# Kernel optimization log

Measured on AMD Instinct MI355X. Metric: run time of the kernel, lower is better.

Reference implementation:

```python
import jax, jax.numpy as jnp
import numpy as np

TEMP = 0.05            # self.temp
NUM_INSTANCES = 16     # self.num_instances


def _l2norm(x):
    return x / jnp.linalg.norm(x, axis=-1, keepdims=True)


def setup_inputs() -> dict:
    key = jax.random.key(0)
    ks = jax.random.split(key, 6)
    B, D, N, K, NDATA = 256, 2048, 32768, 8192, 100000
    inputs = jax.random.normal(ks[0], (B, D), jnp.float32)
    # memory bank rows are kept unit-norm by the momentum update; init normalized
    features = _l2norm(jax.random.normal(ks[1], (N, D), jnp.float32))
    kmeans_centeroids = jax.random.normal(ks[2], (K, D), jnp.float32)
    targets = jax.random.randint(ks[3], (B,), 0, N)
    kmeans_pids = jax.random.randint(ks[4], (NDATA,), 0, K)
    indexes = jax.random.randint(ks[5], (B,), 0, NDATA)
    return {"inputs": inputs, "features": features,
            "kmeans_centeroids": kmeans_centeroids, "targets": targets,
            "kmeans_pids": kmeans_pids, "indexes": indexes, "neg_size": 20}


def reference(inputs, features, kmeans_centeroids, targets, kmeans_pids,
              indexes, neg_size):
    B = inputs.shape[0]
    K = kmeans_centeroids.shape[0]
    x = _l2norm(inputs)                                   # F.normalize(inputs, dim=1)
    outputs = x @ features.T                              # CM.forward: [B, N]
    finch_pos = jnp.take_along_axis(outputs, targets[:, None], axis=1)  # [B,1]
    kmeans_score = x @ kmeans_centeroids.T                # [B, K]
    batch_kmeans_pids = kmeans_pids[indexes]              # [B]
    # scatter_(-2) own kmeans cluster, then take top-neg_size negatives
    masked = jax.lax.stop_gradient(kmeans_score)          # detach().clone()
    masked = masked.at[jnp.arange(B), batch_kmeans_pids].set(-2.0)
    _, sel_ind_neg = jax.lax.top_k(masked, neg_size)      # [B, neg_size]
    kmeans_chosen_neg = jnp.take_along_axis(kmeans_score, sel_ind_neg, axis=1)
    mixed_score = jnp.concatenate([finch_pos, kmeans_chosen_neg], axis=1) / TEMP
    # confidence mask: per group of NUM_INSTANCES (first half of batch),
    # sample agrees with the group's modal kmeans pid (np.bincount().argmax())
    half = B // 2
    g = batch_kmeans_pids[:half].reshape(-1, NUM_INSTANCES)        # [G, I]
    counts = jax.nn.one_hot(g, K, dtype=jnp.int32).sum(axis=1)     # [G, K]
    mode = jnp.argmax(counts, axis=1)                              # ties -> smallest id
    mask_half = (g == mode[:, None]).reshape(-1).astype(jnp.float32)
    confidence_mask = jnp.concatenate([mask_half, mask_half])      # [B]
    # CE(mixed_score, 0) per-sample, confidence-weighted mean
    ce_neg = -jax.nn.log_softmax(mixed_score, axis=1)[:, 0]
    neg_con_loss = (confidence_mask * ce_neg).mean()
    # CE(outputs/temp, targets) mean
    logp = jax.nn.log_softmax(outputs / TEMP, axis=1)
    ce_main = -jnp.take_along_axis(logp, targets[:, None], axis=1).mean()
    return 0.2 * neg_con_loss + ce_main
```

## Files before the change

kernel.cpp:

```cpp
#include <hip/hip_runtime.h>
#include <stdint.h>

typedef __attribute__((ext_vector_type(8))) short short8;
typedef __attribute__((ext_vector_type(4))) float floatx4;

__device__ __forceinline__ unsigned short f2b(float f) {
    union { float f; uint32_t u; } v; v.f = f;
    uint32_t u = v.u;
    return (unsigned short)((u + 0x7FFFu + ((u >> 16) & 1u)) >> 16);
}

__device__ __forceinline__ uint32_t pk2(float a, float b) {
    union { float f; uint32_t u; } x, y; x.f = a; y.f = b;
    uint32_t ua = x.u + 0x8000u, ub = y.u + 0x8000u;
    return (ua >> 16) | (ub & 0xFFFF0000u);
}

__device__ __forceinline__ void async16(const void* g, void* l) {
    __builtin_amdgcn_global_load_lds(
        (const __attribute__((address_space(1))) void*)g,
        (__attribute__((address_space(3))) void*)l, 16, 0, 0);
}

__global__ void norm_kernel(const float* __restrict__ in,
                            unsigned short* __restrict__ xb, int D) {
    int b = blockIdx.x, t = threadIdx.x;
    const float* row = in + (size_t)b * D;
    float ss = 0.f;
    for (int i = t * 4; i < D; i += 1024) {
        float4 v = *(const float4*)(row + i);
        ss += v.x * v.x + v.y * v.y + v.z * v.z + v.w * v.w;
    }
    for (int off = 32; off > 0; off >>= 1) ss += __shfl_down(ss, off);
    __shared__ float wsum[4];
    __shared__ float rn_sh;
    if ((t & 63) == 0) wsum[t >> 6] = ss;
    __syncthreads();
    if (t == 0) rn_sh = rsqrtf(wsum[0] + wsum[1] + wsum[2] + wsum[3]);
    __syncthreads();
    float rn = rn_sh;
    unsigned short* orow = xb + (size_t)b * D;
    for (int i = t * 4; i < D; i += 1024) {
        float4 v = *(const float4*)(row + i);
        ushort4 o;
        o.x = f2b(v.x * rn); o.y = f2b(v.y * rn);
        o.z = f2b(v.z * rn); o.w = f2b(v.w * rn);
        *(ushort4*)(orow + i) = o;
    }
}

#define BKk 64
__global__ __launch_bounds__(256, 2)
void gemm_kernel(const unsigned short* __restrict__ xb,
                 const float* __restrict__ featB,
                 const float* __restrict__ centB,
                 const int* __restrict__ targets,
                 float* __restrict__ S, float* __restrict__ pos,
                 float* __restrict__ km,
                 int D, int K, int nbF) {
    __shared__ __align__(16) unsigned short Alds[256 * BKk];
    __shared__ __align__(16) unsigned short Blds[64 * BKk];

    const int t = threadIdx.x;
    const int w = t >> 6, l = t & 63;
    const bool isFeat = ((int)blockIdx.x < nbF);
    const int n0 = (isFeat ? (int)blockIdx.x : ((int)blockIdx.x - nbF)) * 64;
    const float* Bsrc = isFeat ? featB : centB;

    floatx4 acc[4][4];
#pragma unroll
    for (int ti = 0; ti < 4; ++ti)
#pragma unroll
        for (int tj = 0; tj < 4; ++tj)
            acc[ti][tj] = (floatx4){0.f, 0.f, 0.f, 0.f};

    const int kIters = D / BKk;
    const int brow = t >> 2, bq = t & 3;
    const float* bg0 = Bsrc + (size_t)(n0 + brow) * D + bq * 16;
    const int bc0 = ((bq * 2) ^ (brow & 7)) * 16;
    const int bc1 = ((bq * 2 + 1) ^ (brow & 7)) * 16;
    const char* xbB = (const char*)xb;

    for (int kt = 0; kt < kIters; ++kt) {
#pragma unroll
        for (int j = 0; j < 8; ++j) {
            int slin = j * 256 + t;
            int r = slin >> 3;
            int cg = (slin & 7) ^ (r & 7);
            async16(xbB + (size_t)r * (D * 2) + kt * (BKk * 2) + cg * 16,
                    (char*)Alds + slin * 16);
        }
        {
            const float* bg = bg0 + kt * BKk;
            float4 f0 = *(const float4*)(bg);
            float4 f1 = *(const float4*)(bg + 4);
            float4 f2 = *(const float4*)(bg + 8);
            float4 f3 = *(const float4*)(bg + 12);
            uint4 p0, p1;
            p0.x = pk2(f0.x, f0.y); p0.y = pk2(f0.z, f0.w);
            p0.z = pk2(f1.x, f1.y); p0.w = pk2(f1.z, f1.w);
            p1.x = pk2(f2.x, f2.y); p1.y = pk2(f2.z, f2.w);
            p1.z = pk2(f3.x, f3.y); p1.w = pk2(f3.z, f3.w);
            char* bb = (char*)Blds + brow * 128;
            *(uint4*)(bb + bc0) = p0;
            *(uint4*)(bb + bc1) = p1;
        }
        __syncthreads();

#pragma unroll
        for (int s = 0; s < 2; ++s) {
            short8 aF[4], bF[4];
#pragma unroll
            for (int ti = 0; ti < 4; ++ti) {
                int R = w * 64 + ti * 16 + (l & 15);
                int g = s * 4 + (l >> 4);
                aF[ti] = *(const short8*)((const char*)Alds +
                          R * 128 + ((g ^ (R & 7)) * 16));
            }
#pragma unroll
            for (int tj = 0; tj < 4; ++tj) {
                int Rn = tj * 16 + (l & 15);
                int g = s * 4 + (l >> 4);
                bF[tj] = *(const short8*)((const char*)Blds +
                          Rn * 128 + ((g ^ (Rn & 7)) * 16));
            }
#pragma unroll
            for (int ti = 0; ti < 4; ++ti)
#pragma unroll
                for (int tj = 0; tj < 4; ++tj)
                    acc[ti][tj] = __builtin_amdgcn_mfma_f32_16x16x32_bf16(
                        aF[ti], bF[tj], acc[ti][tj], 0, 0, 0);
        }
        __syncthreads();
    }

    if (isFeat) {
#pragma unroll
        for (int ti = 0; ti < 4; ++ti) {
#pragma unroll
            for (int r = 0; r < 4; ++r) {
                int row = w * 64 + ti * 16 + ((l >> 4) << 2) + r;
                int tr = targets[row];
                int col0 = n0 + (l & 15);
                float e = 0.f;
#pragma unroll
                for (int tj = 0; tj < 4; ++tj) {
                    float c = acc[ti][tj][r];
                    e += __expf(c * 20.0f);
                    if (tr == col0 + tj * 16) pos[row] = c;
                }
                e += __shfl_xor(e, 1); e += __shfl_xor(e, 2);
                e += __shfl_xor(e, 4); e += __shfl_xor(e, 8);
                if ((l & 15) == 0) atomicAdd(&S[row], e);
            }
        }
    } else {
#pragma unroll
        for (int ti = 0; ti < 4; ++ti) {
#pragma unroll
            for (int r = 0; r < 4; ++r) {
                int row = w * 64 + ti * 16 + ((l >> 4) << 2) + r;
                size_t base = (size_t)row * K + n0 + (l & 15);
#pragma unroll
                for (int tj = 0; tj < 4; ++tj)
                    km[base + tj * 16] = acc[ti][tj][r];
            }
        }
    }
}

__global__ __launch_bounds__(256, 4)
void topk_kernel(const float* __restrict__ kmr,
                 const int* __restrict__ pids,
                 const int* __restrict__ idxs,
                 const int* __restrict__ negsz,
                 float* __restrict__ topv, int K) {
    int b = blockIdx.x, t = threadIdx.x;
    int w = t >> 6, l = t & 63;
    const float* row = kmr + (size_t)b * K;
    float v[32];
#pragma unroll
    for (int k = 0; k < 32; ++k) v[k] = row[k * 256 + t];
    int gi = pids[idxs[b]];
    if ((gi & 255) == t) {
        int kk = gi >> 8;
#pragma unroll
        for (int k = 0; k < 32; ++k) if (k == kk) v[k] = -1e30f;
    }
    float bv = v[0]; int bk = 0;
#pragma unroll
    for (int k = 1; k < 32; ++k) if (v[k] > bv) { bv = v[k]; bk = k; }

    __shared__ float rv[4];
    __shared__ int rg[4];
    int ns = *negsz; if (ns > 32) ns = 32;
    for (int j = 0; j < ns; ++j) {
        float mv = bv; int mg = bk * 256 + t;
#pragma unroll
        for (int off = 1; off < 64; off <<= 1) {
            float ov = __shfl_xor(mv, off);
            int og = __shfl_xor(mg, off);
            if (ov > mv) { mv = ov; mg = og; }
        }
        if (l == 0) { rv[w] = mv; rg[w] = mg; }
        __syncthreads();
        float gv = rv[0]; int gg = rg[0];
#pragma unroll
        for (int ww = 1; ww < 4; ++ww)
            if (rv[ww] > gv) { gv = rv[ww]; gg = rg[ww]; }
        if (t == 0) topv[b * 32 + j] = gv;
        if ((gg & 255) == t) {
            int kk = gg >> 8;
#pragma unroll
            for (int k = 0; k < 32; ++k) if (k == kk) v[k] = -1e30f;
            bv = v[0]; bk = 0;
#pragma unroll
            for (int k = 1; k < 32; ++k) if (v[k] > bv) { bv = v[k]; bk = k; }
        }
        __syncthreads();
    }
}

__global__ void final_kernel(const float* __restrict__ S,
                             const float* __restrict__ pos,
                             const float* __restrict__ topv,
                             const int* __restrict__ pids,
                             const int* __restrict__ idxs,
                             const int* __restrict__ negsz,
                             float* __restrict__ out, int B) {
    __shared__ int pid_sh[256];
    __shared__ int mode_sh[16];
    __shared__ float red[256];
    int t = threadIdx.x;
    if (t < B) pid_sh[t] = pids[idxs[t]];
    __syncthreads();
    int half = B >> 1;
    int G = half / 16;
    if (t < G) {
        int bestPid = 0x7FFFFFFF, bestCnt = -1;
        for (int i = 0; i < 16; ++i) {
            int p = pid_sh[t * 16 + i];
            int c = 0;
            for (int j = 0; j < 16; ++j) c += (pid_sh[t * 16 + j] == p) ? 1 : 0;
            if (c > bestCnt || (c == bestCnt && p < bestPid)) { bestCnt = c; bestPid = p; }
        }
        mode_sh[t] = bestPid;
    }
    __syncthreads();
    float contrib = 0.f;
    if (t < B) {
        int hb = (t < half) ? t : t - half;
        float mask = (pid_sh[hb] == mode_sh[hb / 16]) ? 1.f : 0.f;
        int ns = *negsz; if (ns > 32) ns = 32;
        float p20 = pos[t] * 20.0f;
        float m = p20;
        for (int j = 0; j < ns; ++j) m = fmaxf(m, topv[t * 32 + j] * 20.0f);
        float se = __expf(p20 - m);
        for (int j = 0; j < ns; ++j) se += __expf(topv[t * 32 + j] * 20.0f - m);
        float ce_neg = m + logf(se) - p20;
        float ce_main = logf(S[t]) - p20;
        contrib = (0.2f * mask * ce_neg + ce_main) / (float)B;
    }
    red[t] = contrib;
    __syncthreads();
    for (int s = 128; s > 0; s >>= 1) {
        if (t < s) red[t] += red[t + s];
        __syncthreads();
    }
    if (t == 0) out[0] = red[0];
}

extern "C" void kernel_launch(void* const* d_in, const int* in_sizes, int n_in,
                              void* d_out, int out_size, void* d_ws, size_t ws_size,
                              hipStream_t stream) {
    const float* inputs   = (const float*)d_in[0];
    const float* features = (const float*)d_in[1];
    const float* cents    = (const float*)d_in[2];
    const int*   targets  = (const int*)d_in[3];
    const int*   pids     = (const int*)d_in[4];
    const int*   idxs     = (const int*)d_in[5];
    const int*   negsz    = (const int*)d_in[6];
    float* out = (float*)d_out;

    int Bb = in_sizes[3];
    int Dd = in_sizes[0] / Bb;
    int Nn = in_sizes[1] / Dd;
    int Kk = in_sizes[2] / Dd;

    char* ws = (char*)d_ws;
    unsigned short* xb = (unsigned short*)ws;
    size_t o = (size_t)Bb * Dd * 2;
    float* km   = (float*)(ws + o); o += (size_t)Bb * Kk * 4;
    float* S    = (float*)(ws + o); o += (size_t)Bb * 4;
    float* pos  = (float*)(ws + o); o += (size_t)Bb * 4;
    float* topv = (float*)(ws + o); o += (size_t)Bb * 32 * 4;

    hipMemsetAsync(S, 0, (size_t)Bb * 4, stream);
    norm_kernel<<<Bb, 256, 0, stream>>>(inputs, xb, Dd);
    int nbF = Nn / 64, nbC = Kk / 64;
    gemm_kernel<<<nbF + nbC, 256, 0, stream>>>(xb, features, cents, targets,
                                               S, pos, km, Dd, Kk, nbF);
    topk_kernel<<<Bb, 256, 0, stream>>>(km, pids, idxs, negsz, topv, Kk);
    final_kernel<<<1, 256, 0, stream>>>(S, pos, topv, pids, idxs, negsz, out, Bb);
}
```

Baseline: 490.4 us.

## Double-buffer GEMM LDS tiles to overlap next-tile loads with MFMA compute

Splits the A and B shared-memory tiles into two buffers. The kernel issues the async A load and the global fp32 B load for tile k+1 before running the MFMAs on tile k, and packs and stores B afterwards. This hides global-load latency behind compute and cuts one barrier per iteration. LDS use doubles to about 80KB per block, which may conflict with the launch bound of 2 blocks per CU and lower occupancy.

```diff
diff --git a/kernel.cpp b/kernel.cpp
--- a/kernel.cpp
+++ b/kernel.cpp
@@ -58,8 +58,8 @@
                  float* __restrict__ S, float* __restrict__ pos,
                  float* __restrict__ km,
                  int D, int K, int nbF) {
-    __shared__ __align__(16) unsigned short Alds[256 * BKk];
-    __shared__ __align__(16) unsigned short Blds[64 * BKk];
+    __shared__ __align__(16) unsigned short Alds[2][256 * BKk];
+    __shared__ __align__(16) unsigned short Blds[2][64 * BKk];
 
     const int t = threadIdx.x;
     const int w = t >> 6, l = t & 63;
@@ -81,32 +81,20 @@
     const int bc1 = ((bq * 2 + 1) ^ (brow & 7)) * 16;
     const char* xbB = (const char*)xb;
 
-    for (int kt = 0; kt < kIters; ++kt) {
+    auto stageA = [&](int nb, int ktn) {
 #pragma unroll
         for (int j = 0; j < 8; ++j) {
             int slin = j * 256 + t;
             int r = slin >> 3;
             int cg = (slin & 7) ^ (r & 7);
-            async16(xbB + (size_t)r * (D * 2) + kt * (BKk * 2) + cg * 16,
-                    (char*)Alds + slin * 16);
-        }
-        {
-            const float* bg = bg0 + kt * BKk;
-            float4 f0 = *(const float4*)(bg);
-            float4 f1 = *(const float4*)(bg + 4);
-            float4 f2 = *(const float4*)(bg + 8);
-            float4 f3 = *(const float4*)(bg + 12);
-            uint4 p0, p1;
-            p0.x = pk2(f0.x, f0.y); p0.y = pk2(f0.z, f0.w);
-            p0.z = pk2(f1.x, f1.y); p0.w = pk2(f1.z, f1.w);
-            p1.x = pk2(f2.x, f2.y); p1.y = pk2(f2.z, f2.w);
-            p1.z = pk2(f3.x, f3.y); p1.w = pk2(f3.z, f3.w);
-            char* bb = (char*)Blds + brow * 128;
-            *(uint4*)(bb + bc0) = p0;
-            *(uint4*)(bb + bc1) = p1;
-        }
-        __syncthreads();
-
+            async16(xbB + (size_t)r * (D * 2) + (size_t)ktn * (BKk * 2) + cg * 16,
+                    (char*)(&Alds[nb][0]) + slin * 16);
+        }
+    };
+
+    auto compute = [&](int cb) {
+        const char* Ab = (const char*)(&Alds[cb][0]);
+        const char* Bb = (const char*)(&Blds[cb][0]);
 #pragma unroll
         for (int s = 0; s < 2; ++s) {
             short8 aF[4], bF[4];
@@ -114,15 +102,13 @@
             for (int ti = 0; ti < 4; ++ti) {
                 int R = w * 64 + ti * 16 + (l & 15);
                 int g = s * 4 + (l >> 4);
-                aF[ti] = *(const short8*)((const char*)Alds +
-                          R * 128 + ((g ^ (R & 7)) * 16));
+                aF[ti] = *(const short8*)(Ab + R * 128 + ((g ^ (R & 7)) * 16));
             }
 #pragma unroll
             for (int tj = 0; tj < 4; ++tj) {
                 int Rn = tj * 16 + (l & 15);
                 int g = s * 4 + (l >> 4);
-                bF[tj] = *(const short8*)((const char*)Blds +
-                          Rn * 128 + ((g ^ (Rn & 7)) * 16));
+                bF[tj] = *(const short8*)(Bb + Rn * 128 + ((g ^ (Rn & 7)) * 16));
             }
 #pragma unroll
             for (int ti = 0; ti < 4; ++ti)
@@ -131,8 +117,48 @@
                     acc[ti][tj] = __builtin_amdgcn_mfma_f32_16x16x32_bf16(
                         aF[ti], bF[tj], acc[ti][tj], 0, 0, 0);
         }
+    };
+
+    stageA(0, 0);
+    {
+        const float* bg = bg0;
+        float4 f0 = *(const float4*)(bg);
+        float4 f1 = *(const float4*)(bg + 4);
+        float4 f2 = *(const float4*)(bg + 8);
+        float4 f3 = *(const float4*)(bg + 12);
+        uint4 p0, p1;
+        p0.x = pk2(f0.x, f0.y); p0.y = pk2(f0.z, f0.w);
+        p0.z = pk2(f1.x, f1.y); p0.w = pk2(f1.z, f1.w);
+        p1.x = pk2(f2.x, f2.y); p1.y = pk2(f2.z, f2.w);
+        p1.z = pk2(f3.x, f3.y); p1.w = pk2(f3.z, f3.w);
+        char* bb = (char*)(&Blds[0][0]) + brow * 128;
+        *(uint4*)(bb + bc0) = p0;
+        *(uint4*)(bb + bc1) = p1;
+    }
+    __syncthreads();
+
+    for (int kt = 0; kt < kIters - 1; ++kt) {
+        const int cb = kt & 1, nb = cb ^ 1;
+        stageA(nb, kt + 1);
+        const float* bg = bg0 + (kt + 1) * BKk;
+        float4 f0 = *(const float4*)(bg);
+        float4 f1 = *(const float4*)(bg + 4);
+        float4 f2 = *(const float4*)(bg + 8);
+        float4 f3 = *(const float4*)(bg + 12);
+
+        compute(cb);
+
+        uint4 p0, p1;
+        p0.x = pk2(f0.x, f0.y); p0.y = pk2(f0.z, f0.w);
+        p0.z = pk2(f1.x, f1.y); p0.w = pk2(f1.z, f1.w);
+        p1.x = pk2(f2.x, f2.y); p1.y = pk2(f2.z, f2.w);
+        p1.z = pk2(f3.x, f3.y); p1.w = pk2(f3.z, f3.w);
+        char* bb = (char*)(&Blds[nb][0]) + brow * 128;
+        *(uint4*)(bb + bc0) = p0;
+        *(uint4*)(bb + bc1) = p1;
         __syncthreads();
     }
+    compute((kIters - 1) & 1);
 
     if (isFeat) {
 #pragma unroll
```

New measurement: 549.7 us. +12.1%, slower.

## Read A fragments directly from global, enlarge K tile, stage only B in LDS

Applied to the files above, without the earlier changes.

The GEMM no longer stages the normalized bf16 input tile in LDS through async global-to-LDS loads. Each wave now loads its A fragments straight from global memory (relying on L2/L1 caching, since every block reads the same 256xD input). The K tile grows from 64 to 256, so there are fewer barriers per block, and occupancy is raised to 3 blocks per SIMD-group because LDS use drops. The cost is uncoalesced, latency-exposed global loads for A inside the MFMA loop, with nothing prefetched to overlap them.

```diff
diff --git a/kernel.cpp b/kernel.cpp
--- a/kernel.cpp
+++ b/kernel.cpp
@@ -14,12 +14,6 @@
     union { float f; uint32_t u; } x, y; x.f = a; y.f = b;
     uint32_t ua = x.u + 0x8000u, ub = y.u + 0x8000u;
     return (ua >> 16) | (ub & 0xFFFF0000u);
-}
-
-__device__ __forceinline__ void async16(const void* g, void* l) {
-    __builtin_amdgcn_global_load_lds(
-        (const __attribute__((address_space(1))) void*)g,
-        (__attribute__((address_space(3))) void*)l, 16, 0, 0);
 }
 
 __global__ void norm_kernel(const float* __restrict__ in,
@@ -49,8 +43,8 @@
     }
 }
 
-#define BKk 64
-__global__ __launch_bounds__(256, 2)
+#define BKk 256
+__global__ __launch_bounds__(256, 3)
 void gemm_kernel(const unsigned short* __restrict__ xb,
                  const float* __restrict__ featB,
                  const float* __restrict__ centB,
@@ -58,11 +52,11 @@
                  float* __restrict__ S, float* __restrict__ pos,
                  float* __restrict__ km,
                  int D, int K, int nbF) {
-    __shared__ __align__(16) unsigned short Alds[256 * BKk];
     __shared__ __align__(16) unsigned short Blds[64 * BKk];
 
     const int t = threadIdx.x;
     const int w = t >> 6, l = t & 63;
+    const int lo = l & 15, hi = l >> 4;
     const bool isFeat = ((int)blockIdx.x < nbF);
     const int n0 = (isFeat ? (int)blockIdx.x : ((int)blockIdx.x - nbF)) * 64;
     const float* Bsrc = isFeat ? featB : centB;
@@ -75,54 +69,41 @@
             acc[ti][tj] = (floatx4){0.f, 0.f, 0.f, 0.f};
 
     const int kIters = D / BKk;
-    const int brow = t >> 2, bq = t & 3;
-    const float* bg0 = Bsrc + (size_t)(n0 + brow) * D + bq * 16;
-    const int bc0 = ((bq * 2) ^ (brow & 7)) * 16;
-    const int bc1 = ((bq * 2 + 1) ^ (brow & 7)) * 16;
     const char* xbB = (const char*)xb;
 
+    const int bcc   = t & 31;
+    const int brow0 = t >> 5;
+    const int bslot = (bcc ^ (brow0 & 7)) * 16;
+    const float* bgbase = Bsrc + (size_t)(n0 + brow0) * D + bcc * 8;
+
     for (int kt = 0; kt < kIters; ++kt) {
 #pragma unroll
         for (int j = 0; j < 8; ++j) {
-            int slin = j * 256 + t;
-            int r = slin >> 3;
-            int cg = (slin & 7) ^ (r & 7);
-            async16(xbB + (size_t)r * (D * 2) + kt * (BKk * 2) + cg * 16,
-                    (char*)Alds + slin * 16);
-        }
-        {
-            const float* bg = bg0 + kt * BKk;
-            float4 f0 = *(const float4*)(bg);
-            float4 f1 = *(const float4*)(bg + 4);
-            float4 f2 = *(const float4*)(bg + 8);
-            float4 f3 = *(const float4*)(bg + 12);
-            uint4 p0, p1;
-            p0.x = pk2(f0.x, f0.y); p0.y = pk2(f0.z, f0.w);
-            p0.z = pk2(f1.x, f1.y); p0.w = pk2(f1.z, f1.w);
-            p1.x = pk2(f2.x, f2.y); p1.y = pk2(f2.z, f2.w);
-            p1.z = pk2(f3.x, f3.y); p1.w = pk2(f3.z, f3.w);
-            char* bb = (char*)Blds + brow * 128;
-            *(uint4*)(bb + bc0) = p0;
-            *(uint4*)(bb + bc1) = p1;
-        }
-        __syncthreads();
-
-#pragma unroll
-        for (int s = 0; s < 2; ++s) {
+            const float* src = bgbase + (size_t)j * 8 * D + kt * BKk;
+            float4 fa = *(const float4*)(src);
+            float4 fb = *(const float4*)(src + 4);
+            uint4 p;
+            p.x = pk2(fa.x, fa.y); p.y = pk2(fa.z, fa.w);
+            p.z = pk2(fb.x, fb.y); p.w = pk2(fb.z, fb.w);
+            *(uint4*)((char*)Blds + (j * 8 + brow0) * 512 + bslot) = p;
+        }
+        __syncthreads();
+
+#pragma unroll
+        for (int kk = 0; kk < 8; ++kk) {
             short8 aF[4], bF[4];
 #pragma unroll
             for (int ti = 0; ti < 4; ++ti) {
-                int R = w * 64 + ti * 16 + (l & 15);
-                int g = s * 4 + (l >> 4);
-                aF[ti] = *(const short8*)((const char*)Alds +
-                          R * 128 + ((g ^ (R & 7)) * 16));
+                int R = w * 64 + ti * 16 + lo;
+                aF[ti] = *(const short8*)(xbB + (size_t)R * (D * 2)
+                          + kt * (BKk * 2) + kk * 64 + hi * 16);
             }
 #pragma unroll
             for (int tj = 0; tj < 4; ++tj) {
-                int Rn = tj * 16 + (l & 15);
-                int g = s * 4 + (l >> 4);
+                int Rn = tj * 16 + lo;
+                int chunk = kk * 4 + hi;
                 bF[tj] = *(const short8*)((const char*)Blds +
-                          Rn * 128 + ((g ^ (Rn & 7)) * 16));
+                          Rn * 512 + ((chunk ^ (Rn & 7)) * 16));
             }
 #pragma unroll
             for (int ti = 0; ti < 4; ++ti)
```

Measured after the change: 538.7 us. 1.1x slower.
